# Performance work log

Measured on AMD Instinct MI355X. Metric: run time of the kernel, lower is better.

## Reference

```python
import jax, jax.numpy as jnp
import numpy as np

SR = 16000.0          # sample_rate
L = 512               # wavetable_length


def setup_inputs() -> dict:
    key = jax.random.key(0)
    k0, k1 = jax.random.split(key)
    # f0: [B, 1, T] fundamental-frequency contour in Hz (~50..490 Hz)
    f0 = jax.random.uniform(k0, (8, 1, 64000), dtype=jnp.float32) * 440.0 + 50.0
    # learned wavetable parameter [1, L, n_wavetables, 1], sine-initialised
    idx = jnp.cumsum(jnp.ones((L, 1), dtype=jnp.float32), axis=0)
    wavetable = jnp.sin(2.0 * jnp.pi * idx / L)[None, :, :, None]
    return {"f0": f0, "wavetable": wavetable}


def reference(f0, wavetable):
    # phase: [B, 1, 1, T] in [0, 1)
    phase = (jnp.cumsum(f0, axis=-1) / SR)[:, :, None, :] % 1.0
    # wt_phase: [1, L, 1, 1]
    wt_phase = jnp.linspace(0.0, 1.0, L, dtype=f0.dtype)[None, :, None, None]
    # diff/weights: [B, L, n_wt, T] -- the dense 2-point linear-interp weights
    diff = jnp.abs(phase - wt_phase) * L
    weights = jax.nn.relu(1.0 - diff)
    # weighted sum over wavetable axis -> [B, n_wt, T]
    return (wavetable * weights).sum(axis=1)
```

## Files before the change

### kernel.cpp

```cpp
#include <hip/hip_runtime.h>


#define BPR 32
#define TPB 1024

__device__ __forceinline__ float interp_emit(double run, const float* __restrict__ wt,
                                             float Lm1, float inv_Lm1, float Lf, int imax) {
  double x = run * (1.0 / 16000.0);
  float ph = (float)(x - floor(x));
  float pos = ph * Lm1;
  int i0 = (int)pos;
  i0 = (i0 > imax) ? imax : i0;
  float wtp0 = (float)i0 * inv_Lm1;
  float wtp1 = (float)(i0 + 1) * inv_Lm1;
  float w0 = fmaxf(0.0f, 1.0f - fabsf(ph - wtp0) * Lf);
  float w1 = fmaxf(0.0f, 1.0f - fabsf(ph - wtp1) * Lf);
  return wt[i0] * w0 + wt[i0 + 1] * w1;
}

__global__ __launch_bounds__(TPB) void wavetable_onepass_kernel(
    const float* __restrict__ f0, const float* __restrict__ wt,
    float* __restrict__ out, int T, int L) {
  const int r = blockIdx.x / BPR;
  const int b = blockIdx.x % BPR;
  const int t = threadIdx.x;
  const int E = T / BPR;
  const int base = b * E;
  const int lane = t & 63, wid = t >> 6;

  const float* __restrict__ src = f0 + (size_t)r * T;
  float* __restrict__ dst = out + (size_t)r * T;

  __shared__ double lds[TPB / 64];

  double pre = 0.0;
  {
    const int n4 = base >> 2;
    const float4* __restrict__ s4 = (const float4*)src;
    for (int k = t; k < n4; k += TPB) {
      float4 x = s4[k];
      pre += (double)x.x + (double)x.y + (double)x.z + (double)x.w;
    }
    #pragma unroll
    for (int d = 1; d < 64; d <<= 1) pre += __shfl_xor(pre, d, 64);
    if (lane == 0) lds[wid] = pre;
    __syncthreads();
    double tot = 0.0;
    #pragma unroll
    for (int w = 0; w < TPB / 64; ++w) tot += lds[w];
    pre = tot;
    __syncthreads();
  }

  const int myi = base + t * 2;
  const bool act = (t * 2 < E);
  float x0 = 0.0f, x1 = 0.0f;
  if (act) {
    float2 v = *(const float2*)(src + myi);
    x0 = v.x; x1 = v.y;
  }
  double s = (double)x0 + (double)x1;
  double incl = s;
  #pragma unroll
  for (int d = 1; d < 64; d <<= 1) {
    double u = __shfl_up(incl, d, 64);
    if (lane >= d) incl += u;
  }
  if (lane == 63) lds[wid] = incl;
  __syncthreads();
  double woff = 0.0;
  for (int w = 0; w < wid; ++w) woff += lds[w];
  double run = pre + woff + (incl - s);

  if (act) {
    const float Lm1 = (float)(L - 1);
    const float inv_Lm1 = 1.0f / Lm1;
    const float Lf = (float)L;
    const int imax = L - 2;
    double r0 = run + (double)x0;
    double r1 = r0 + (double)x1;
    float2 o;
    o.x = interp_emit(r0, wt, Lm1, inv_Lm1, Lf, imax);
    o.y = interp_emit(r1, wt, Lm1, inv_Lm1, Lf, imax);
    *(float2*)(dst + myi) = o;
  }
}

#define THREADS 512
__global__ __launch_bounds__(THREADS) void wavetable_fused_kernel(
    const float* __restrict__ f0, const float* __restrict__ wt,
    float* __restrict__ out, int T, int L) {
  const int r = blockIdx.x;
  const int t = threadIdx.x;
  const int chunk = (T + THREADS - 1) / THREADS;
  const int beg = t * chunk;
  const int end = (beg + chunk < T) ? (beg + chunk) : T;
  const float* __restrict__ src = f0 + (size_t)r * T;
  float* __restrict__ dst = out + (size_t)r * T;
  double s = 0.0;
  for (int k = beg; k < end; ++k) s += (double)src[k];
  double v = s;
  const int lane = t & 63, wid = t >> 6;
  #pragma unroll
  for (int d = 1; d < 64; d <<= 1) {
    double u = __shfl_up(v, d, 64);
    if (lane >= d) v += u;
  }
  __shared__ double wsum[THREADS / 64];
  if (lane == 63) wsum[wid] = v;
  __syncthreads();
  if (t == 0) {
    double acc = 0.0;
    #pragma unroll
    for (int w = 0; w < THREADS / 64; ++w) { double tmp = wsum[w]; wsum[w] = acc; acc += tmp; }
  }
  __syncthreads();
  double run = wsum[wid] + (v - s);
  const float Lm1 = (float)(L - 1);
  const float inv_Lm1 = 1.0f / Lm1;
  const float Lf = (float)L;
  const int imax = L - 2;
  for (int k = beg; k < end; ++k) {
    run += (double)src[k];
    double x = run * (1.0 / 16000.0);
    float ph = (float)(x - floor(x));
    float pos = ph * Lm1;
    int i0 = (int)pos;
    i0 = (i0 > imax) ? imax : i0;
    float wtp0 = (float)i0 * inv_Lm1;
    float wtp1 = (float)(i0 + 1) * inv_Lm1;
    float w0 = fmaxf(0.0f, 1.0f - fabsf(ph - wtp0) * Lf);
    float w1 = fmaxf(0.0f, 1.0f - fabsf(ph - wtp1) * Lf);
    dst[k] = wt[i0] * w0 + wt[i0 + 1] * w1;
  }
}

extern "C" void kernel_launch(void* const* d_in, const int* in_sizes, int n_in,
                              void* d_out, int out_size, void* d_ws, size_t ws_size,
                              hipStream_t stream) {
  const float* f0 = (const float*)d_in[0];
  const float* wt = (const float*)d_in[1];
  float* out = (float*)d_out;

  const int total = in_sizes[0];
  const int L = in_sizes[1];
  const int rows = 8;
  const int T = total / rows;

  if (total == rows * T && (T % (BPR * 4)) == 0 && (T / BPR) <= 2 * TPB &&
      ((T / BPR) & 1) == 0) {
    wavetable_onepass_kernel<<<rows * BPR, TPB, 0, stream>>>(f0, wt, out, T, L);
  } else {
    wavetable_fused_kernel<<<rows, THREADS, 0, stream>>>(f0, wt, out, T, L);
  }
}
```

Measured before the change: 11.05 us.

## Split one-pass scan into slice-sum kernel plus scan-emit kernel

Replaces the single kernel, where each block re-reads all preceding elements of its row to compute its prefix, with a two-kernel reduce-then-scan. The first kernel writes per-slice sums to workspace. The second kernel gets each block's prefix by a wavefront reduction over the earlier slice sums. This removes the quadratic redundant prefix reads, at the cost of an extra launch and a round trip through global memory.

```diff
diff --git a/kernel.cpp b/kernel.cpp
--- a/kernel.cpp
+++ b/kernel.cpp
@@ -3,6 +3,33 @@
 
 #define BPR 32
 #define TPB 1024
+
+__global__ __launch_bounds__(TPB) void slice_sum_kernel(
+    const float* __restrict__ f0, double* __restrict__ ssum, int E) {
+  const int blk = blockIdx.x;
+  const int t = threadIdx.x;
+  const int lane = t & 63, wid = t >> 6;
+  const float* __restrict__ src = f0 + (size_t)blk * E;
+
+  double s = 0.0;
+  const int i = t * 2;
+  if (i < E) {
+    float2 v = *(const float2*)(src + i);
+    s = (double)v.x + (double)v.y;
+  }
+  #pragma unroll
+  for (int d = 1; d < 64; d <<= 1) s += __shfl_xor(s, d, 64);
+
+  __shared__ double lds[TPB / 64];
+  if (lane == 0) lds[wid] = s;
+  __syncthreads();
+  if (t == 0) {
+    double tot = 0.0;
+    #pragma unroll
+    for (int w = 0; w < TPB / 64; ++w) tot += lds[w];
+    ssum[blk] = tot;
+  }
+}
 
 __device__ __forceinline__ float interp_emit(double run, const float* __restrict__ wt,
                                              float Lm1, float inv_Lm1, float Lf, int imax) {
@@ -18,47 +45,27 @@
   return wt[i0] * w0 + wt[i0 + 1] * w1;
 }
 
-__global__ __launch_bounds__(TPB) void wavetable_onepass_kernel(
-    const float* __restrict__ f0, const float* __restrict__ wt,
-    float* __restrict__ out, int T, int L) {
-  const int r = blockIdx.x / BPR;
-  const int b = blockIdx.x % BPR;
+__global__ __launch_bounds__(TPB) void scan_emit_kernel(
+    const float* __restrict__ f0, const double* __restrict__ ssum,
+    const float* __restrict__ wt, float* __restrict__ out, int E, int L) {
+  const int blk = blockIdx.x;
+  const int b = blk & (BPR - 1);
   const int t = threadIdx.x;
-  const int E = T / BPR;
-  const int base = b * E;
   const int lane = t & 63, wid = t >> 6;
+  const size_t base = (size_t)blk * E;
 
-  const float* __restrict__ src = f0 + (size_t)r * T;
-  float* __restrict__ dst = out + (size_t)r * T;
-
-  __shared__ double lds[TPB / 64];
-
-  double pre = 0.0;
-  {
-    const int n4 = base >> 2;
-    const float4* __restrict__ s4 = (const float4*)src;
-    for (int k = t; k < n4; k += TPB) {
-      float4 x = s4[k];
-      pre += (double)x.x + (double)x.y + (double)x.z + (double)x.w;
-    }
-    #pragma unroll
-    for (int d = 1; d < 64; d <<= 1) pre += __shfl_xor(pre, d, 64);
-    if (lane == 0) lds[wid] = pre;
-    __syncthreads();
-    double tot = 0.0;
-    #pragma unroll
-    for (int w = 0; w < TPB / 64; ++w) tot += lds[w];
-    pre = tot;
-    __syncthreads();
+  const int i = t * 2;
+  const bool act = (i < E);
+  float x0 = 0.0f, x1 = 0.0f;
+  if (act) {
+    float2 v = *(const float2*)(f0 + base + i);
+    x0 = v.x; x1 = v.y;
   }
 
-  const int myi = base + t * 2;
-  const bool act = (t * 2 < E);
-  float x0 = 0.0f, x1 = 0.0f;
-  if (act) {
-    float2 v = *(const float2*)(src + myi);
-    x0 = v.x; x1 = v.y;
-  }
+  double pre = (lane < b) ? ssum[(blk - b) + lane] : 0.0;
+  #pragma unroll
+  for (int d = 1; d < 64; d <<= 1) pre += __shfl_xor(pre, d, 64);
+
   double s = (double)x0 + (double)x1;
   double incl = s;
   #pragma unroll
@@ -66,10 +73,11 @@
     double u = __shfl_up(incl, d, 64);
     if (lane >= d) incl += u;
   }
-  if (lane == 63) lds[wid] = incl;
+  __shared__ double wtot[TPB / 64];
+  if (lane == 63) wtot[wid] = incl;
   __syncthreads();
   double woff = 0.0;
-  for (int w = 0; w < wid; ++w) woff += lds[w];
+  for (int w = 0; w < wid; ++w) woff += wtot[w];
   double run = pre + woff + (incl - s);
 
   if (act) {
@@ -82,7 +90,7 @@
     float2 o;
     o.x = interp_emit(r0, wt, Lm1, inv_Lm1, Lf, imax);
     o.y = interp_emit(r1, wt, Lm1, inv_Lm1, Lf, imax);
-    *(float2*)(dst + myi) = o;
+    *(float2*)(out + base + i) = o;
   }
 }
 
@@ -146,10 +154,15 @@
   const int L = in_sizes[1];
   const int rows = 8;
   const int T = total / rows;
+  const int E = T / BPR;
+  const int nblk = rows * BPR;
 
-  if (total == rows * T && (T % (BPR * 4)) == 0 && (T / BPR) <= 2 * TPB &&
-      ((T / BPR) & 1) == 0) {
-    wavetable_onepass_kernel<<<rows * BPR, TPB, 0, stream>>>(f0, wt, out, T, L);
+  const size_t need = (size_t)nblk * sizeof(double);
+  if (total == rows * T && (T % BPR) == 0 && (E & 1) == 0 &&
+      E <= 2 * TPB && ws_size >= need && BPR <= 32) {
+    double* ssum = (double*)d_ws;
+    slice_sum_kernel<<<nblk, TPB, 0, stream>>>(f0, ssum, E);
+    scan_emit_kernel<<<nblk, TPB, 0, stream>>>(f0, ssum, wt, out, E, L);
   } else {
     wavetable_fused_kernel<<<rows, THREADS, 0, stream>>>(f0, wt, out, T, L);
   }
```

After: 13.61 us. 23.2% more time.
